# Kernel optimization log

Hardware: AMD Instinct MI355X
Metric: run time of the kernel (lower is better)

## Reference

```python
import jax, jax.numpy as jnp
import numpy as np

B = 8192          # batch rows
C_IN = 4096       # total input channels
G = 8             # number of clusters
CG = C_IN // G    # channels per cluster (arrangement.shape[0])
J = 512           # j_rank per cluster (output width per cluster)


def setup_inputs() -> dict:
    key = jax.random.key(0)
    kx, kp, kw, kb = jax.random.split(key, 4)
    x = jax.random.normal(kx, (B, C_IN), dtype=jnp.float32)
    # arrangements: a random permutation of all input channels split into G groups,
    # mimicking channel-clustering assignments (each channel used exactly once)
    perm = jax.random.permutation(kp, C_IN)
    arrangements = perm.reshape(G, CG).astype(jnp.int64)
    # per-group nn.Linear weights: torch layout (out_features, in_features)
    weights = jax.random.normal(kw, (G, J, CG), dtype=jnp.float32) * (1.0 / np.sqrt(CG))
    bias = jax.random.normal(kb, (G, J), dtype=jnp.float32) * 0.02
    return {"x": x, "arrangements": arrangements, "weights": weights, "bias": bias}


def reference(x, arrangements, weights, bias):
    # Gather each cluster's channels: x[:, arrangements] -> [B, G, CG]
    xg = jnp.take(x, arrangements, axis=1)
    # Per-group linear (torch Linear: y = x @ W.T + b), batched over groups,
    # then concat along feature dim -> [B, G*J]
    out = jnp.einsum('bgc,gjc->bgj', xg, weights) + bias[None, :, :]
    return out.reshape(x.shape[0], -1)
```

## Files before the change

kernel.cpp:

```cpp
#include <hip/hip_runtime.h>
#include <hip/hip_bf16.h>

#define B_ROWS 8192
#define C_IN   4096
#define G_GRP  8
#define CG     512
#define J_RANK 512

#define BM 128
#define BN 256
#define BK 32
#define NKT (CG / BK)

#define RPB    8
#define PERM_BLOCKS (B_ROWS / RPB)

typedef __attribute__((ext_vector_type(8))) short bf16x8;
typedef __attribute__((ext_vector_type(4))) float f32x4;
typedef __attribute__((ext_vector_type(8))) unsigned short u16x8;

struct ushort4v { unsigned short x, y, z, w; };

__device__ __forceinline__ unsigned short f2bf(float f) {
    unsigned int u = __float_as_uint(f);
    unsigned int r = (u + 0x7FFFu + ((u >> 16) & 1u)) >> 16;
    return (unsigned short)r;
}

__global__ __launch_bounds__(256) void convert_w_kernel(
    const float* __restrict__ w, unsigned short* __restrict__ wb, int n4) {
    int i = blockIdx.x * 256 + threadIdx.x;
    if (i >= n4) return;
    float4 v = ((const float4*)w)[i];
    ushort4v o;
    o.x = f2bf(v.x); o.y = f2bf(v.y); o.z = f2bf(v.z); o.w = f2bf(v.w);
    ((ushort4v*)wb)[i] = o;
}

__global__ __launch_bounds__(256) void permute_x_kernel(
    const float* __restrict__ x, const int* __restrict__ arr,
    unsigned short* __restrict__ xp) {
    __shared__ float buf[3][C_IN];
    const int tid  = threadIdx.x;
    const int row0 = blockIdx.x * RPB;

    const bool is64 = (arr[1] == 0 && arr[3] == 0 && arr[5] == 0 && arr[7] == 0);

    int sidx[16];
#pragma unroll
    for (int pass = 0; pass < 2; ++pass)
#pragma unroll
        for (int k = 0; k < 8; ++k) {
            int p = pass * 2048 + tid * 8 + k;
            sidx[pass * 8 + k] = is64 ? arr[2 * p] : arr[p];
        }

#define PSTAGE(bufi, r)                                                      \
    do {                                                                     \
        const float* src_ = x + (size_t)(row0 + (r)) * C_IN;                 \
        _Pragma("unroll")                                                    \
        for (int i_ = 0; i_ < 4; ++i_) {                                     \
            int c_ = i_ * 256 + tid;                                         \
            __builtin_amdgcn_global_load_lds(                                \
                (const __attribute__((address_space(1))) unsigned int*)      \
                    (src_ + c_ * 4),                                         \
                (__attribute__((address_space(3))) unsigned int*)            \
                    (&buf[bufi][0] + c_ * 4),                                \
                16, 0, 0);                                                   \
        }                                                                    \
    } while (0)

    PSTAGE(0, 0);
    PSTAGE(1, 1);
    PSTAGE(2, 2);

#pragma unroll
    for (int r = 0; r < RPB; ++r) {
        if (r == 0)            asm volatile("s_waitcnt vmcnt(8)"  ::: "memory");
        else if (r == 1)       asm volatile("s_waitcnt vmcnt(10)" ::: "memory");
        else if (r == RPB - 2) asm volatile("s_waitcnt vmcnt(8)"  ::: "memory");
        else if (r == RPB - 1) asm volatile("s_waitcnt vmcnt(4)"  ::: "memory");
        else                   asm volatile("s_waitcnt vmcnt(12)" ::: "memory");
        __builtin_amdgcn_s_barrier();
        __builtin_amdgcn_sched_barrier(0);

        const int bi = r % 3;
        unsigned short* orow = xp + (size_t)(row0 + r) * C_IN;
#pragma unroll
        for (int pass = 0; pass < 2; ++pass) {
            u16x8 o;
#pragma unroll
            for (int k = 0; k < 8; ++k)
                o[k] = f2bf(buf[bi][sidx[pass * 8 + k]]);
            *(u16x8*)(orow + pass * 2048 + tid * 8) = o;
        }

        __builtin_amdgcn_sched_barrier(0);
        __builtin_amdgcn_s_barrier();
        if (r + 3 < RPB) PSTAGE(bi, r + 3);
    }
#undef PSTAGE
}

__global__ __launch_bounds__(512, 4) void gemm_kernel(
    const unsigned short* __restrict__ Xp,
    const unsigned short* __restrict__ Wb,
    const float* __restrict__ bias,
    float* __restrict__ out) {
    __shared__ unsigned short ldsA[3][BM * BK];
    __shared__ unsigned short ldsB[2][BN * BK];

    const int tid = threadIdx.x;
    const int g   = blockIdx.x & 7;
    const int idx = blockIdx.x >> 3;
    const int mt  = idx >> 1;
    const int nt  = idx & 1;

    const int l   = tid & 63;
    const int wv  = tid >> 6;
    const int wr  = wv >> 2;
    const int wc  = wv & 3;
    const int lr  = l & 15;
    const int lkq = l >> 4;

    const unsigned short* Ab = Xp + (size_t)(mt * BM) * C_IN + g * CG;
    const unsigned short* Bb = Wb + (size_t)g * J_RANK * CG + (size_t)(nt * BN) * CG;

    f32x4 acc[4][4];
#pragma unroll
    for (int m = 0; m < 4; ++m)
#pragma unroll
        for (int n = 0; n < 4; ++n) acc[m][n] = (f32x4){0.f, 0.f, 0.f, 0.f};

    const int coff = (lkq ^ ((lr >> 2) & 3)) * 8;

#define STAGE_A(kt_)                                                          \
    do { const int p_ = (kt_) % 3;                                            \
        int c_ = tid;                                                         \
        int rl_ = c_ >> 2, gc_ = (c_ & 3) ^ ((rl_ >> 2) & 3);                 \
        __builtin_amdgcn_global_load_lds(                                     \
            (const __attribute__((address_space(1))) unsigned int*)           \
                (Ab + (size_t)rl_ * C_IN + (kt_) * BK + gc_ * 8),             \
            (__attribute__((address_space(3))) unsigned int*)                 \
                (&ldsA[p_][0] + c_ * 8),                                      \
            16, 0, 0);                                                        \
    } while (0)

#define STAGE_B(kt_)                                                          \
    do { const int p_ = (kt_) & 1;                                            \
        _Pragma("unroll")                                                     \
        for (int i_ = 0; i_ < 2; ++i_) {                                      \
            int c_ = i_ * 512 + tid;                                          \
            int rl_ = c_ >> 2, gc_ = (c_ & 3) ^ ((rl_ >> 2) & 3);             \
            __builtin_amdgcn_global_load_lds(                                 \
                (const __attribute__((address_space(1))) unsigned int*)       \
                    (Bb + (size_t)rl_ * CG + (kt_) * BK + gc_ * 8),           \
                (__attribute__((address_space(3))) unsigned int*)             \
                    (&ldsB[p_][0] + c_ * 8),                                  \
                16, 0, 0);                                                    \
        }                                                                     \
    } while (0)

#define LDA(m_) (*(const bf16x8*)&ldsA[bufA][(wr * 64 + (m_) * 16 + lr) * BK + coff])
#define LDB(n_) (*(const bf16x8*)&ldsB[bufB][(wc * 64 + (n_) * 16 + lr) * BK + coff])

#define PHASE_TAIL()                                                          \
    __builtin_amdgcn_s_barrier();                                             \
    asm volatile("s_waitcnt lgkmcnt(0)" ::: "memory");                        \
    __builtin_amdgcn_sched_barrier(0);                                        \
    __builtin_amdgcn_s_setprio(1)

#define PHASE_END()                                                           \
    __builtin_amdgcn_s_setprio(0);                                            \
    __builtin_amdgcn_s_barrier()

    STAGE_A(0); STAGE_B(0);
    STAGE_A(1); STAGE_B(1);
    asm volatile("s_waitcnt vmcnt(3)" ::: "memory");
    __builtin_amdgcn_s_barrier();

    bf16x8 bfr[4], af[2];

    for (int kt = 0; kt < NKT; ++kt) {
        const int bufA = kt % 3;
        const int bufB = kt & 1;

#pragma unroll
        for (int n = 0; n < 4; ++n) bfr[n] = LDB(n);
        af[0] = LDA(0); af[1] = LDA(1);
        if (kt + 2 < NKT) STAGE_A(kt + 2);
        PHASE_TAIL();
#pragma unroll
        for (int mm = 0; mm < 2; ++mm)
#pragma unroll
            for (int n = 0; n < 4; ++n)
                acc[mm][n] = __builtin_amdgcn_mfma_f32_16x16x32_bf16(
                    af[mm], bfr[n], acc[mm][n], 0, 0, 0);
        PHASE_END();

        af[0] = LDA(2); af[1] = LDA(3);
        if (kt + 2 < NKT) STAGE_B(kt + 2);
        if (kt <= NKT - 3)      asm volatile("s_waitcnt vmcnt(3)" ::: "memory");
        else if (kt == NKT - 2) asm volatile("s_waitcnt vmcnt(0)" ::: "memory");
        PHASE_TAIL();
#pragma unroll
        for (int mm = 0; mm < 2; ++mm)
#pragma unroll
            for (int n = 0; n < 4; ++n)
                acc[2 + mm][n] = __builtin_amdgcn_mfma_f32_16x16x32_bf16(
                    af[mm], bfr[n], acc[2 + mm][n], 0, 0, 0);
        PHASE_END();
    }
#undef STAGE_A
#undef STAGE_B
#undef LDA
#undef LDB
#undef PHASE_TAIL
#undef PHASE_END

    const int r0 = mt * BM + wr * 64 + (lkq << 2);
    const int cbase = nt * BN + wc * 64 + lr;
#pragma unroll
    for (int n = 0; n < 4; ++n) {
        int col = cbase + n * 16;
        float bv = bias[g * J_RANK + col];
#pragma unroll
        for (int m = 0; m < 4; ++m) {
            int row = r0 + m * 16;
            float* op = out + (size_t)row * C_IN + g * J_RANK + col;
#pragma unroll
            for (int r = 0; r < 4; ++r)
                op[(size_t)r * C_IN] = acc[m][n][r] + bv;
        }
    }
}

extern "C" void kernel_launch(void* const* d_in, const int* in_sizes, int n_in,
                              void* d_out, int out_size, void* d_ws, size_t ws_size,
                              hipStream_t stream) {
    const float* x    = (const float*)d_in[0];
    const int*   arr  = (const int*)d_in[1];
    const float* w    = (const float*)d_in[2];
    const float* bias = (const float*)d_in[3];
    float* out = (float*)d_out;

    unsigned short* xp = (unsigned short*)d_ws;
    unsigned short* wb = xp + (size_t)B_ROWS * C_IN;

    hipLaunchKernelGGL(convert_w_kernel, dim3((G_GRP * J_RANK * CG / 4 + 255) / 256),
                       dim3(256), 0, stream, w, wb, G_GRP * J_RANK * CG / 4);
    hipLaunchKernelGGL(permute_x_kernel, dim3(PERM_BLOCKS), dim3(256), 0, stream,
                       x, arr, xp);
    hipLaunchKernelGGL(gemm_kernel,
                       dim3(G_GRP * (B_ROWS / BM) * (J_RANK / BN)), dim3(512),
                       0, stream, xp, wb, bias, out);
}
```

Before: 105.9 us.

## Restructure permute kernel to per-wave row ownership without block barriers

```diff
diff --git a/kernel.cpp b/kernel.cpp
--- a/kernel.cpp
+++ b/kernel.cpp
@@ -12,8 +12,9 @@
 #define BK 32
 #define NKT (CG / BK)
 
-#define RPB    8
-#define PERM_BLOCKS (B_ROWS / RPB)
+#define PW_WAVES 8
+#define PW_RPW   4
+#define PW_BLOCKS (B_ROWS / (PW_WAVES * PW_RPW))
 
 typedef __attribute__((ext_vector_type(8))) short bf16x8;
 typedef __attribute__((ext_vector_type(4))) float f32x4;
@@ -37,69 +38,54 @@
     ((ushort4v*)wb)[i] = o;
 }
 
-__global__ __launch_bounds__(256) void permute_x_kernel(
+__global__ __launch_bounds__(512, 2) void permute_x_kernel(
     const float* __restrict__ x, const int* __restrict__ arr,
     unsigned short* __restrict__ xp) {
-    __shared__ float buf[3][C_IN];
-    const int tid  = threadIdx.x;
-    const int row0 = blockIdx.x * RPB;
+    __shared__ float slice_all[PW_WAVES][C_IN];
+    const int tid = threadIdx.x;
+    const int w   = tid >> 6;
+    const int l   = tid & 63;
+    float* slice = &slice_all[w][0];
+    const int row0 = blockIdx.x * (PW_WAVES * PW_RPW) + w * PW_RPW;
 
     const bool is64 = (arr[1] == 0 && arr[3] == 0 && arr[5] == 0 && arr[7] == 0);
 
-    int sidx[16];
-#pragma unroll
-    for (int pass = 0; pass < 2; ++pass)
-#pragma unroll
-        for (int k = 0; k < 8; ++k) {
-            int p = pass * 2048 + tid * 8 + k;
-            sidx[pass * 8 + k] = is64 ? arr[2 * p] : arr[p];
-        }
-
-#define PSTAGE(bufi, r)                                                      \
-    do {                                                                     \
-        const float* src_ = x + (size_t)(row0 + (r)) * C_IN;                 \
-        _Pragma("unroll")                                                    \
-        for (int i_ = 0; i_ < 4; ++i_) {                                     \
-            int c_ = i_ * 256 + tid;                                         \
-            __builtin_amdgcn_global_load_lds(                                \
-                (const __attribute__((address_space(1))) unsigned int*)      \
-                    (src_ + c_ * 4),                                         \
-                (__attribute__((address_space(3))) unsigned int*)            \
-                    (&buf[bufi][0] + c_ * 4),                                \
-                16, 0, 0);                                                   \
-        }                                                                    \
-    } while (0)
-
-    PSTAGE(0, 0);
-    PSTAGE(1, 1);
-    PSTAGE(2, 2);
-
-#pragma unroll
-    for (int r = 0; r < RPB; ++r) {
-        if (r == 0)            asm volatile("s_waitcnt vmcnt(8)"  ::: "memory");
-        else if (r == 1)       asm volatile("s_waitcnt vmcnt(10)" ::: "memory");
-        else if (r == RPB - 2) asm volatile("s_waitcnt vmcnt(8)"  ::: "memory");
-        else if (r == RPB - 1) asm volatile("s_waitcnt vmcnt(4)"  ::: "memory");
-        else                   asm volatile("s_waitcnt vmcnt(12)" ::: "memory");
-        __builtin_amdgcn_s_barrier();
+    int sidx[64];
+#pragma unroll
+    for (int c = 0; c < 8; ++c)
+#pragma unroll
+        for (int j = 0; j < 8; ++j) {
+            int p = c * 512 + l * 8 + j;
+            sidx[c * 8 + j] = is64 ? arr[2 * p] : arr[p];
+        }
+
+#pragma unroll
+    for (int r = 0; r < PW_RPW; ++r) {
+        const float* xrow = x + (size_t)(row0 + r) * C_IN;
+#pragma unroll
+        for (int i = 0; i < 16; ++i) {
+            __builtin_amdgcn_global_load_lds(
+                (const __attribute__((address_space(1))) unsigned int*)
+                    (xrow + i * 256 + l * 4),
+                (__attribute__((address_space(3))) unsigned int*)
+                    (slice + i * 256 + l * 4),
+                16, 0, 0);
+        }
+        asm volatile("s_waitcnt vmcnt(0)" ::: "memory");
         __builtin_amdgcn_sched_barrier(0);
 
-        const int bi = r % 3;
         unsigned short* orow = xp + (size_t)(row0 + r) * C_IN;
 #pragma unroll
-        for (int pass = 0; pass < 2; ++pass) {
+        for (int c = 0; c < 8; ++c) {
             u16x8 o;
 #pragma unroll
-            for (int k = 0; k < 8; ++k)
-                o[k] = f2bf(buf[bi][sidx[pass * 8 + k]]);
-            *(u16x8*)(orow + pass * 2048 + tid * 8) = o;
-        }
-
+            for (int j = 0; j < 8; ++j)
+                o[j] = f2bf(slice[sidx[c * 8 + j]]);
+            *(u16x8*)(orow + c * 512 + l * 8) = o;
+        }
+        asm volatile("s_waitcnt lgkmcnt(0)" ::: "memory");
         __builtin_amdgcn_sched_barrier(0);
-        __builtin_amdgcn_s_barrier();
-        if (r + 3 < RPB) PSTAGE(bi, r + 3);
     }
-#undef PSTAGE
 }
 
 __global__ __launch_bounds__(512, 4) void gemm_kernel(
@@ -249,7 +235,7 @@
 
     hipLaunchKernelGGL(convert_w_kernel, dim3((G_GRP * J_RANK * CG / 4 + 255) / 256),
                        dim3(256), 0, stream, w, wb, G_GRP * J_RANK * CG / 4);
-    hipLaunchKernelGGL(permute_x_kernel, dim3(PERM_BLOCKS), dim3(256), 0, stream,
+    hipLaunchKernelGGL(permute_x_kernel, dim3(PW_BLOCKS), dim3(512), 0, stream,
                        x, arr, xp);
     hipLaunchKernelGGL(gemm_kernel,
                        dim3(G_GRP * (B_ROWS / BM) * (J_RANK / BN)), dim3(512),
```

Result: slower. 115.9 us (+9.4%).
